# Kernel optimization log

Measured on AMD Instinct MI355X. Metric: run time of the kernel, lower is better.

Reference implementation:

```python
import jax, jax.numpy as jnp
import numpy as np

B, C = 65536, 1000
EPS = float(np.finfo(np.float32).eps)

def setup_inputs() -> dict:
    key = jax.random.key(0)
    k1, k2, k3 = jax.random.split(key, 3)
    return {
        "Simple_vector": jax.random.normal(k1, (B, C), dtype=jnp.float32),
        "label_list": jax.random.randint(k2, (B,), 0, C),
        "w_L": jax.random.normal(k3, (C,), dtype=jnp.float32),
        "w_H": jnp.ones((1,), dtype=jnp.float32),
        "b": jnp.ones((1,), dtype=jnp.float32),
    }

def reference(Simple_vector, label_list, w_L, w_H, b):
    C_ = Simple_vector.shape[1]
    # LTS: per-row dot with class-weight vector
    LTS = Simple_vector @ w_L  # (B,)
    # H_hat = sum_i p_i * log p_i  (negative entropy), single stable pass
    logp = jax.nn.log_softmax(Simple_vector, axis=1)
    H_hat = jnp.sum(jnp.exp(logp) * logp, axis=1)  # (B,)
    HTS = w_H[0] * (H_hat / jnp.log(jnp.float32(C_))) + b[0]
    a = LTS + HTS
    T = jnp.clip(jax.nn.softplus(a), EPS, None)  # (B,)
    scaled = Simple_vector / T[:, None]
    # mean cross-entropy
    ls = jax.nn.log_softmax(scaled, axis=1)
    nll = -jnp.take_along_axis(ls, label_list[:, None], axis=1)[:, 0]
    return jnp.mean(nll)
```

## Files before the change

### kernel.cpp

```cpp
#include <hip/hip_runtime.h>
#include <float.h>
#include <math.h>


static constexpr int   kC4    = 250;
static constexpr int   kBlock = 256;
static constexpr int   kGrid  = 2048;
static constexpr int   kWavesTotal = kGrid * (kBlock / 64);
static constexpr int   kRPW   = 8;
static constexpr float kEps   = 1.1920928955078125e-07f;
static constexpr float kLogC  = 6.907755279f;

__device__ __forceinline__ float wred_max(float v) {
#pragma unroll
  for (int off = 32; off > 0; off >>= 1) v = fmaxf(v, __shfl_xor(v, off, 64));
  return v;
}
__device__ __forceinline__ float wred_sum(float v) {
#pragma unroll
  for (int off = 32; off > 0; off >>= 1) v += __shfl_xor(v, off, 64);
  return v;
}

__device__ __forceinline__ void p1_dot_max(const float4 c, const float4 w,
                                           float& L, float& m) {
  L = fmaf(c.x, w.x, L); L = fmaf(c.y, w.y, L);
  L = fmaf(c.z, w.z, L); L = fmaf(c.w, w.w, L);
  m = fmaxf(m, fmaxf(fmaxf(c.x, c.y), fmaxf(c.z, c.w)));
}
__device__ __forceinline__ void p2_sumexp(const float4 c, const float m,
                                          float& S, float& W) {
  float e;
  e = __expf(c.x - m); S += e; W = fmaf(e, c.x, W);
  e = __expf(c.y - m); S += e; W = fmaf(e, c.y, W);
  e = __expf(c.z - m); S += e; W = fmaf(e, c.z, W);
  e = __expf(c.w - m); S += e; W = fmaf(e, c.w, W);
}
__device__ __forceinline__ void p3_sumexp2(const float4 c, const float rT,
                                           const float nmrT, float& S2) {
  S2 += __expf(fmaf(c.x, rT, nmrT)); S2 += __expf(fmaf(c.y, rT, nmrT));
  S2 += __expf(fmaf(c.z, rT, nmrT)); S2 += __expf(fmaf(c.w, rT, nmrT));
}

#define SENT4 make_float4(-FLT_MAX, -FLT_MAX, -FLT_MAX, -FLT_MAX)

__device__ __forceinline__ float row_nll(
    const float4 c0, const float4 c1, const float4 c2, const float4 c3,
    const float4 w0, const float4 w1, const float4 w2, const float4 w3,
    const int labc, const float wH0, const float b0) {
  float L = 0.f, m = -FLT_MAX;
  p1_dot_max(c0, w0, L, m); p1_dot_max(c1, w1, L, m);
  p1_dot_max(c2, w2, L, m); p1_dot_max(c3, w3, L, m);
  m = wred_max(m);

  float S = 0.f, W = 0.f;
  p2_sumexp(c0, m, S, W); p2_sumexp(c1, m, S, W);
  p2_sumexp(c2, m, S, W); p2_sumexp(c3, m, S, W);
  S = wred_sum(S);
  W = wred_sum(W);
  L = wred_sum(L);

  const int c4l = labc >> 2;
  const int sl  = c4l >> 6, ln = c4l & 63, el = labc & 3;
  float4 v = (sl == 0) ? c0 : (sl == 1) ? c1 : (sl == 2) ? c2 : c3;
  float cand = (el == 0) ? v.x : (el == 1) ? v.y : (el == 2) ? v.z : v.w;
  const float xl = __shfl(cand, ln, 64);

  const float Hhat = W / S - m - __logf(S);
  const float a    = L + wH0 * (Hhat / kLogC) + b0;
  const float sp   = (a > 0.f) ? (a + log1pf(__expf(-a))) : log1pf(__expf(a));
  const float T    = fmaxf(sp, kEps);
  const float rT   = 1.0f / T;
  const float nmrT = -m * rT;

  float S2 = 0.f;
  p3_sumexp2(c0, rT, nmrT, S2); p3_sumexp2(c1, rT, nmrT, S2);
  p3_sumexp2(c2, rT, nmrT, S2); p3_sumexp2(c3, rT, nmrT, S2);
  S2 = wred_sum(S2);

  return __logf(S2) - fmaf(xl, rT, nmrT);
}

__global__ __launch_bounds__(kBlock) void ats_row_kernel_c8(
    const float* __restrict__ X, const int* __restrict__ labels,
    const float* __restrict__ wL, const float* __restrict__ wH,
    const float* __restrict__ bb, double* __restrict__ partial) {
  const int lane   = threadIdx.x & 63;
  const int wib    = threadIdx.x >> 6;
  const int wid    = blockIdx.x * (kBlock / 64) + wib;
  const bool tailok = lane < (kC4 - 192);

  const float4* WLr = reinterpret_cast<const float4*>(wL);
  const float4 w0 = WLr[lane];
  const float4 w1 = WLr[64 + lane];
  const float4 w2 = WLr[128 + lane];
  const float4 w3 = tailok ? WLr[192 + lane] : make_float4(0.f, 0.f, 0.f, 0.f);
  const float wH0 = wH[0];
  const float b0  = bb[0];

  double acc = 0.0;
  const int base = wid * kRPW;

  float4 c0, c1, c2, c3;
  int labc;
  {
    const float4* Xr = reinterpret_cast<const float4*>(X) + (size_t)base * kC4;
    c0 = Xr[lane]; c1 = Xr[64 + lane]; c2 = Xr[128 + lane];
    c3 = tailok ? Xr[192 + lane] : SENT4;
    labc = labels[base];
  }

  for (int i = 0; i < kRPW; ++i) {
    float4 n0 = SENT4, n1 = SENT4, n2 = SENT4, n3 = SENT4;
    int labn = 0;
    if (i + 1 < kRPW) {
      const float4* Xn =
          reinterpret_cast<const float4*>(X) + (size_t)(base + i + 1) * kC4;
      n0 = Xn[lane]; n1 = Xn[64 + lane]; n2 = Xn[128 + lane];
      n3 = tailok ? Xn[192 + lane] : SENT4;
      labn = labels[base + i + 1];
    }

    acc += (double)row_nll(c0, c1, c2, c3, w0, w1, w2, w3, labc, wH0, b0);

    c0 = n0; c1 = n1; c2 = n2; c3 = n3; labc = labn;
  }

  __shared__ double sacc[kBlock / 64];
  if (lane == 0) sacc[wib] = acc;
  __syncthreads();
  if (threadIdx.x == 0)
    partial[blockIdx.x] = (sacc[0] + sacc[1]) + (sacc[2] + sacc[3]);
}

__global__ __launch_bounds__(kBlock) void ats_row_kernel_gen(
    const float* __restrict__ X, const int* __restrict__ labels,
    const float* __restrict__ wL, const float* __restrict__ wH,
    const float* __restrict__ bb, double* __restrict__ partial, int B) {
  const int lane   = threadIdx.x & 63;
  const int wib    = threadIdx.x >> 6;
  const int wid    = blockIdx.x * (kBlock / 64) + wib;
  const bool tailok = lane < (kC4 - 192);

  const float4* WLr = reinterpret_cast<const float4*>(wL);
  const float4 w0 = WLr[lane];
  const float4 w1 = WLr[64 + lane];
  const float4 w2 = WLr[128 + lane];
  const float4 w3 = tailok ? WLr[192 + lane] : make_float4(0.f, 0.f, 0.f, 0.f);
  const float wH0 = wH[0];
  const float b0  = bb[0];

  double acc = 0.0;
  int row = wid;
  float4 c0, c1, c2, c3;
  int labc = 0;
  if (row < B) {
    const float4* Xr = reinterpret_cast<const float4*>(X) + (size_t)row * kC4;
    c0 = Xr[lane]; c1 = Xr[64 + lane]; c2 = Xr[128 + lane];
    c3 = tailok ? Xr[192 + lane] : SENT4;
    labc = labels[row];
  }
  for (; row < B; row += kWavesTotal) {
    const int nrow = row + kWavesTotal;
    float4 n0 = SENT4, n1 = SENT4, n2 = SENT4, n3 = SENT4;
    int labn = 0;
    if (nrow < B) {
      const float4* Xn = reinterpret_cast<const float4*>(X) + (size_t)nrow * kC4;
      n0 = Xn[lane]; n1 = Xn[64 + lane]; n2 = Xn[128 + lane];
      n3 = tailok ? Xn[192 + lane] : SENT4;
      labn = labels[nrow];
    }
    acc += (double)row_nll(c0, c1, c2, c3, w0, w1, w2, w3, labc, wH0, b0);
    c0 = n0; c1 = n1; c2 = n2; c3 = n3; labc = labn;
  }
  __shared__ double sacc[kBlock / 64];
  if (lane == 0) sacc[wib] = acc;
  __syncthreads();
  if (threadIdx.x == 0)
    partial[blockIdx.x] = (sacc[0] + sacc[1]) + (sacc[2] + sacc[3]);
}

__global__ __launch_bounds__(256) void ats_final_kernel(
    const double* __restrict__ partial, float* __restrict__ out, int n, int B) {
  __shared__ double sdata[256];
  double a = 0.0;
  for (int i = threadIdx.x; i < n; i += 256) a += partial[i];
  sdata[threadIdx.x] = a;
  __syncthreads();
#pragma unroll
  for (int s = 128; s > 0; s >>= 1) {
    if ((int)threadIdx.x < s) sdata[threadIdx.x] += sdata[threadIdx.x + s];
    __syncthreads();
  }
  if (threadIdx.x == 0) out[0] = (float)(sdata[0] / (double)B);
}

extern "C" void kernel_launch(void* const* d_in, const int* in_sizes, int n_in,
                              void* d_out, int out_size, void* d_ws, size_t ws_size,
                              hipStream_t stream) {
  (void)n_in; (void)out_size; (void)ws_size;
  const float* X   = (const float*)d_in[0];
  const int*   lab = (const int*)d_in[1];
  const float* wL  = (const float*)d_in[2];
  const float* wH  = (const float*)d_in[3];
  const float* bb  = (const float*)d_in[4];
  const int B = in_sizes[1];
  double* partial = (double*)d_ws;
  float* out = (float*)d_out;

  if (B == kWavesTotal * kRPW) {
    ats_row_kernel_c8<<<kGrid, kBlock, 0, stream>>>(X, lab, wL, wH, bb, partial);
  } else {
    ats_row_kernel_gen<<<kGrid, kBlock, 0, stream>>>(X, lab, wL, wH, bb,
                                                     partial, B);
  }
  ats_final_kernel<<<1, 256, 0, stream>>>(partial, out, kGrid, B);
}
```

Baseline: 63.34 us.

## Fuse final reduction via last-block atomic, use DPP reductions and exp2 math

For the fast path, the final reduction kernel is folded into the row kernel using an atomic counter, so the last block sums the partials, and a memset resets the counter. Wave reductions switch from shuffles to DPP row operations plus readlane. Inputs are prescaled by log2e so the kernel can use native exp2/log2/rcp intrinsics. The generic path loses its prefetch pipelining. The aim is to cut a kernel launch and the shuffle/transcendental instruction cost, at the price of an extra memset launch and slightly different rounding.

```diff
diff --git a/kernel.cpp b/kernel.cpp
--- a/kernel.cpp
+++ b/kernel.cpp
@@ -8,93 +8,106 @@
 static constexpr int   kGrid  = 2048;
 static constexpr int   kWavesTotal = kGrid * (kBlock / 64);
 static constexpr int   kRPW   = 8;
-static constexpr float kEps   = 1.1920928955078125e-07f;
-static constexpr float kLogC  = 6.907755279f;
-
-__device__ __forceinline__ float wred_max(float v) {
-#pragma unroll
-  for (int off = 32; off > 0; off >>= 1) v = fmaxf(v, __shfl_xor(v, off, 64));
-  return v;
-}
-__device__ __forceinline__ float wred_sum(float v) {
-#pragma unroll
-  for (int off = 32; off > 0; off >>= 1) v += __shfl_xor(v, off, 64);
-  return v;
-}
-
-__device__ __forceinline__ void p1_dot_max(const float4 c, const float4 w,
+static constexpr float kEps     = 1.1920928955078125e-07f;
+static constexpr float kInvLogC = 0.14476482730108395f;
+static constexpr float kLn2     = 0.6931471805599453f;
+static constexpr float kLog2e   = 1.4426950408889634f;
+static constexpr float kSent    = -1.7014118e38f;
+
+template <int Ctrl, int Rmask>
+__device__ __forceinline__ float dpp_add(float v) {
+  int t = __builtin_amdgcn_update_dpp(0, __builtin_bit_cast(int, v),
+                                      Ctrl, Rmask, 0xf, false);
+  return v + __builtin_bit_cast(float, t);
+}
+template <int Ctrl, int Rmask>
+__device__ __forceinline__ float dpp_max(float v) {
+  int t = __builtin_amdgcn_update_dpp((int)0xFF800000,
+                                      __builtin_bit_cast(int, v),
+                                      Ctrl, Rmask, 0xf, false);
+  return fmaxf(v, __builtin_bit_cast(float, t));
+}
+__device__ __forceinline__ float bcast63(float v) {
+  return __builtin_bit_cast(
+      float, __builtin_amdgcn_readlane(__builtin_bit_cast(int, v), 63));
+}
+__device__ __forceinline__ float wred_sum_dpp(float v) {
+  v = dpp_add<0xB1, 0xF>(v);
+  v = dpp_add<0x4E, 0xF>(v);
+  v = dpp_add<0x141, 0xF>(v);
+  v = dpp_add<0x140, 0xF>(v);
+  v = dpp_add<0x142, 0xA>(v);
+  v = dpp_add<0x143, 0xC>(v);
+  return bcast63(v);
+}
+__device__ __forceinline__ float wred_max_dpp(float v) {
+  v = dpp_max<0xB1, 0xF>(v);
+  v = dpp_max<0x4E, 0xF>(v);
+  v = dpp_max<0x141, 0xF>(v);
+  v = dpp_max<0x140, 0xF>(v);
+  v = dpp_max<0x142, 0xA>(v);
+  v = dpp_max<0x143, 0xC>(v);
+  return bcast63(v);
+}
+__device__ __forceinline__ void wred_sum3_dpp(float& a, float& b, float& c) {
+  a = dpp_add<0xB1, 0xF>(a);  b = dpp_add<0xB1, 0xF>(b);  c = dpp_add<0xB1, 0xF>(c);
+  a = dpp_add<0x4E, 0xF>(a);  b = dpp_add<0x4E, 0xF>(b);  c = dpp_add<0x4E, 0xF>(c);
+  a = dpp_add<0x141, 0xF>(a); b = dpp_add<0x141, 0xF>(b); c = dpp_add<0x141, 0xF>(c);
+  a = dpp_add<0x140, 0xF>(a); b = dpp_add<0x140, 0xF>(b); c = dpp_add<0x140, 0xF>(c);
+  a = dpp_add<0x142, 0xA>(a); b = dpp_add<0x142, 0xA>(b); c = dpp_add<0x142, 0xA>(c);
+  a = dpp_add<0x143, 0xC>(a); b = dpp_add<0x143, 0xC>(b); c = dpp_add<0x143, 0xC>(c);
+  a = bcast63(a); b = bcast63(b); c = bcast63(c);
+}
+
+__device__ __forceinline__ void scale4(float4& c) {
+  c.x *= kLog2e; c.y *= kLog2e; c.z *= kLog2e; c.w *= kLog2e;
+}
+__device__ __forceinline__ void p1_dot_max(const float4 y, const float4 w,
                                            float& L, float& m) {
-  L = fmaf(c.x, w.x, L); L = fmaf(c.y, w.y, L);
-  L = fmaf(c.z, w.z, L); L = fmaf(c.w, w.w, L);
-  m = fmaxf(m, fmaxf(fmaxf(c.x, c.y), fmaxf(c.z, c.w)));
-}
-__device__ __forceinline__ void p2_sumexp(const float4 c, const float m,
-                                          float& S, float& W) {
+  L = fmaf(y.x, w.x, L); L = fmaf(y.y, w.y, L);
+  L = fmaf(y.z, w.z, L); L = fmaf(y.w, w.w, L);
+  m = fmaxf(m, fmaxf(fmaxf(y.x, y.y), fmaxf(y.z, y.w)));
+}
+__device__ __forceinline__ void p2_sumexp(const float4 y, const float my,
+                                          float& S, float& Wp) {
   float e;
-  e = __expf(c.x - m); S += e; W = fmaf(e, c.x, W);
-  e = __expf(c.y - m); S += e; W = fmaf(e, c.y, W);
-  e = __expf(c.z - m); S += e; W = fmaf(e, c.z, W);
-  e = __expf(c.w - m); S += e; W = fmaf(e, c.w, W);
-}
-__device__ __forceinline__ void p3_sumexp2(const float4 c, const float rT,
-                                           const float nmrT, float& S2) {
-  S2 += __expf(fmaf(c.x, rT, nmrT)); S2 += __expf(fmaf(c.y, rT, nmrT));
-  S2 += __expf(fmaf(c.z, rT, nmrT)); S2 += __expf(fmaf(c.w, rT, nmrT));
-}
-
-#define SENT4 make_float4(-FLT_MAX, -FLT_MAX, -FLT_MAX, -FLT_MAX)
-
-__device__ __forceinline__ float row_nll(
-    const float4 c0, const float4 c1, const float4 c2, const float4 c3,
-    const float4 w0, const float4 w1, const float4 w2, const float4 w3,
-    const int labc, const float wH0, const float b0) {
-  float L = 0.f, m = -FLT_MAX;
-  p1_dot_max(c0, w0, L, m); p1_dot_max(c1, w1, L, m);
-  p1_dot_max(c2, w2, L, m); p1_dot_max(c3, w3, L, m);
-  m = wred_max(m);
-
-  float S = 0.f, W = 0.f;
-  p2_sumexp(c0, m, S, W); p2_sumexp(c1, m, S, W);
-  p2_sumexp(c2, m, S, W); p2_sumexp(c3, m, S, W);
-  S = wred_sum(S);
-  W = wred_sum(W);
-  L = wred_sum(L);
-
-  const int c4l = labc >> 2;
-  const int sl  = c4l >> 6, ln = c4l & 63, el = labc & 3;
-  float4 v = (sl == 0) ? c0 : (sl == 1) ? c1 : (sl == 2) ? c2 : c3;
-  float cand = (el == 0) ? v.x : (el == 1) ? v.y : (el == 2) ? v.z : v.w;
-  const float xl = __shfl(cand, ln, 64);
-
-  const float Hhat = W / S - m - __logf(S);
-  const float a    = L + wH0 * (Hhat / kLogC) + b0;
-  const float sp   = (a > 0.f) ? (a + log1pf(__expf(-a))) : log1pf(__expf(a));
-  const float T    = fmaxf(sp, kEps);
-  const float rT   = 1.0f / T;
-  const float nmrT = -m * rT;
-
-  float S2 = 0.f;
-  p3_sumexp2(c0, rT, nmrT, S2); p3_sumexp2(c1, rT, nmrT, S2);
-  p3_sumexp2(c2, rT, nmrT, S2); p3_sumexp2(c3, rT, nmrT, S2);
-  S2 = wred_sum(S2);
-
-  return __logf(S2) - fmaf(xl, rT, nmrT);
-}
+  e = __builtin_amdgcn_exp2f(y.x - my); S += e; Wp = fmaf(e, y.x, Wp);
+  e = __builtin_amdgcn_exp2f(y.y - my); S += e; Wp = fmaf(e, y.y, Wp);
+  e = __builtin_amdgcn_exp2f(y.z - my); S += e; Wp = fmaf(e, y.z, Wp);
+  e = __builtin_amdgcn_exp2f(y.w - my); S += e; Wp = fmaf(e, y.w, Wp);
+}
+__device__ __forceinline__ void p3_sumexp2(const float4 y, const float rT,
+                                           const float nmy, float& S2) {
+  S2 += __builtin_amdgcn_exp2f(fmaf(y.x, rT, nmy));
+  S2 += __builtin_amdgcn_exp2f(fmaf(y.y, rT, nmy));
+  S2 += __builtin_amdgcn_exp2f(fmaf(y.z, rT, nmy));
+  S2 += __builtin_amdgcn_exp2f(fmaf(y.w, rT, nmy));
+}
+__device__ __forceinline__ float pick_lab(const float4 v, const int el) {
+  return (el == 0) ? v.x : (el == 1) ? v.y : (el == 2) ? v.z : v.w;
+}
+
+#define SENT4 make_float4(kSent, kSent, kSent, kSent)
 
 __global__ __launch_bounds__(kBlock) void ats_row_kernel_c8(
     const float* __restrict__ X, const int* __restrict__ labels,
     const float* __restrict__ wL, const float* __restrict__ wH,
-    const float* __restrict__ bb, double* __restrict__ partial) {
+    const float* __restrict__ bb, double* __restrict__ partial,
+    unsigned* __restrict__ counter, float* __restrict__ out, int B) {
   const int lane   = threadIdx.x & 63;
   const int wib    = threadIdx.x >> 6;
   const int wid    = blockIdx.x * (kBlock / 64) + wib;
   const bool tailok = lane < (kC4 - 192);
 
   const float4* WLr = reinterpret_cast<const float4*>(wL);
-  const float4 w0 = WLr[lane];
-  const float4 w1 = WLr[64 + lane];
-  const float4 w2 = WLr[128 + lane];
-  const float4 w3 = tailok ? WLr[192 + lane] : make_float4(0.f, 0.f, 0.f, 0.f);
+  float4 w0 = WLr[lane];
+  float4 w1 = WLr[64 + lane];
+  float4 w2 = WLr[128 + lane];
+  float4 w3 = tailok ? WLr[192 + lane] : make_float4(0.f, 0.f, 0.f, 0.f);
+  w0.x *= kLn2; w0.y *= kLn2; w0.z *= kLn2; w0.w *= kLn2;
+  w1.x *= kLn2; w1.y *= kLn2; w1.z *= kLn2; w1.w *= kLn2;
+  w2.x *= kLn2; w2.y *= kLn2; w2.z *= kLn2; w2.w *= kLn2;
+  w3.x *= kLn2; w3.y *= kLn2; w3.z *= kLn2; w3.w *= kLn2;
   const float wH0 = wH[0];
   const float b0  = bb[0];
 
@@ -121,18 +134,82 @@
       labn = labels[base + i + 1];
     }
 
-    acc += (double)row_nll(c0, c1, c2, c3, w0, w1, w2, w3, labc, wH0, b0);
+    scale4(c0); scale4(c1); scale4(c2); scale4(c3);
+
+    float L = 0.f, my = -FLT_MAX;
+    p1_dot_max(c0, w0, L, my); p1_dot_max(c1, w1, L, my);
+    p1_dot_max(c2, w2, L, my); p1_dot_max(c3, w3, L, my);
+    my = wred_max_dpp(my);
+
+    float S = 0.f, Wp = 0.f;
+    p2_sumexp(c0, my, S, Wp); p2_sumexp(c1, my, S, Wp);
+    p2_sumexp(c2, my, S, Wp); p2_sumexp(c3, my, S, Wp);
+    wred_sum3_dpp(S, Wp, L);
+
+    const int c4l = labc >> 2;
+    const int sl  = c4l >> 6, ln = c4l & 63, el = labc & 3;
+    float4 v = (sl == 0) ? c0 : (sl == 1) ? c1 : (sl == 2) ? c2 : c3;
+    const float yl = __shfl(pick_lab(v, el), ln, 64);
+
+    const float rcpS = __builtin_amdgcn_rcpf(S);
+    const float Hhat = kLn2 * (Wp * rcpS - my - __builtin_amdgcn_logf(S));
+    const float a    = L + fmaf(wH0, Hhat * kInvLogC, b0);
+    const float sp   = (a > 0.f) ? (a + log1pf(__expf(-a))) : log1pf(__expf(a));
+    const float T    = fmaxf(sp, kEps);
+    const float rT   = __builtin_amdgcn_rcpf(T);
+    const float nmy  = -my * rT;
+
+    float S2 = 0.f;
+    p3_sumexp2(c0, rT, nmy, S2); p3_sumexp2(c1, rT, nmy, S2);
+    p3_sumexp2(c2, rT, nmy, S2); p3_sumexp2(c3, rT, nmy, S2);
+    S2 = wred_sum_dpp(S2);
+
+    const float nll = kLn2 * (__builtin_amdgcn_logf(S2) - fmaf(yl, rT, nmy));
+    acc += (double)nll;
 
     c0 = n0; c1 = n1; c2 = n2; c3 = n3; labc = labn;
   }
 
   __shared__ double sacc[kBlock / 64];
+  __shared__ unsigned slast;
   if (lane == 0) sacc[wib] = acc;
   __syncthreads();
-  if (threadIdx.x == 0)
-    partial[blockIdx.x] = (sacc[0] + sacc[1]) + (sacc[2] + sacc[3]);
-}
-
+  if (threadIdx.x == 0) {
+    const double p = (sacc[0] + sacc[1]) + (sacc[2] + sacc[3]);
+    __hip_atomic_store(&partial[blockIdx.x], p, __ATOMIC_RELEASE,
+                       __HIP_MEMORY_SCOPE_AGENT);
+    const unsigned prev = __hip_atomic_fetch_add(
+        counter, 1u, __ATOMIC_ACQ_REL, __HIP_MEMORY_SCOPE_AGENT);
+    slast = (prev == (unsigned)(gridDim.x - 1)) ? 1u : 0u;
+  }
+  __syncthreads();
+  if (slast) {
+    double a = 0.0;
+    for (int i = threadIdx.x; i < kGrid; i += kBlock)
+      a += __hip_atomic_load(&partial[i], __ATOMIC_RELAXED,
+                             __HIP_MEMORY_SCOPE_AGENT);
+    __shared__ double sred[kBlock];
+    sred[threadIdx.x] = a;
+    __syncthreads();
+#pragma unroll
+    for (int s = kBlock / 2; s > 0; s >>= 1) {
+      if ((int)threadIdx.x < s) sred[threadIdx.x] += sred[threadIdx.x + s];
+      __syncthreads();
+    }
+    if (threadIdx.x == 0) out[0] = (float)(sred[0] / (double)B);
+  }
+}
+
+__device__ __forceinline__ float wred_sum_shfl(float v) {
+#pragma unroll
+  for (int off = 32; off > 0; off >>= 1) v += __shfl_xor(v, off, 64);
+  return v;
+}
+__device__ __forceinline__ float wred_max_shfl(float v) {
+#pragma unroll
+  for (int off = 32; off > 0; off >>= 1) v = fmaxf(v, __shfl_xor(v, off, 64));
+  return v;
+}
 __global__ __launch_bounds__(kBlock) void ats_row_kernel_gen(
     const float* __restrict__ X, const int* __restrict__ labels,
     const float* __restrict__ wL, const float* __restrict__ wH,
@@ -151,27 +228,67 @@
   const float b0  = bb[0];
 
   double acc = 0.0;
-  int row = wid;
-  float4 c0, c1, c2, c3;
-  int labc = 0;
-  if (row < B) {
+  for (int row = wid; row < B; row += kWavesTotal) {
     const float4* Xr = reinterpret_cast<const float4*>(X) + (size_t)row * kC4;
-    c0 = Xr[lane]; c1 = Xr[64 + lane]; c2 = Xr[128 + lane];
-    c3 = tailok ? Xr[192 + lane] : SENT4;
-    labc = labels[row];
-  }
-  for (; row < B; row += kWavesTotal) {
-    const int nrow = row + kWavesTotal;
-    float4 n0 = SENT4, n1 = SENT4, n2 = SENT4, n3 = SENT4;
-    int labn = 0;
-    if (nrow < B) {
-      const float4* Xn = reinterpret_cast<const float4*>(X) + (size_t)nrow * kC4;
-      n0 = Xn[lane]; n1 = Xn[64 + lane]; n2 = Xn[128 + lane];
-      n3 = tailok ? Xn[192 + lane] : SENT4;
-      labn = labels[nrow];
+    float4 c0 = Xr[lane], c1 = Xr[64 + lane], c2 = Xr[128 + lane];
+    float4 c3 = tailok ? Xr[192 + lane] : SENT4;
+    const int labc = labels[row];
+
+    float L = 0.f, m = -FLT_MAX;
+    float S = 0.f, W = 0.f;
+    {
+      float e;
+      L = fmaf(c0.x, w0.x, L); L = fmaf(c0.y, w0.y, L);
+      L = fmaf(c0.z, w0.z, L); L = fmaf(c0.w, w0.w, L);
+      m = fmaxf(m, fmaxf(fmaxf(c0.x, c0.y), fmaxf(c0.z, c0.w)));
+      L = fmaf(c1.x, w1.x, L); L = fmaf(c1.y, w1.y, L);
+      L = fmaf(c1.z, w1.z, L); L = fmaf(c1.w, w1.w, L);
+      m = fmaxf(m, fmaxf(fmaxf(c1.x, c1.y), fmaxf(c1.z, c1.w)));
+      L = fmaf(c2.x, w2.x, L); L = fmaf(c2.y, w2.y, L);
+      L = fmaf(c2.z, w2.z, L); L = fmaf(c2.w, w2.w, L);
+      m = fmaxf(m, fmaxf(fmaxf(c2.x, c2.y), fmaxf(c2.z, c2.w)));
+      L = fmaf(c3.x, w3.x, L); L = fmaf(c3.y, w3.y, L);
+      L = fmaf(c3.z, w3.z, L); L = fmaf(c3.w, w3.w, L);
+      m = fmaxf(m, fmaxf(fmaxf(c3.x, c3.y), fmaxf(c3.z, c3.w)));
+      m = wred_max_shfl(m);
+      e = __expf(c0.x - m); S += e; W = fmaf(e, c0.x, W);
+      e = __expf(c0.y - m); S += e; W = fmaf(e, c0.y, W);
+      e = __expf(c0.z - m); S += e; W = fmaf(e, c0.z, W);
+      e = __expf(c0.w - m); S += e; W = fmaf(e, c0.w, W);
+      e = __expf(c1.x - m); S += e; W = fmaf(e, c1.x, W);
+      e = __expf(c1.y - m); S += e; W = fmaf(e, c1.y, W);
+      e = __expf(c1.z - m); S += e; W = fmaf(e, c1.z, W);
+      e = __expf(c1.w - m); S += e; W = fmaf(e, c1.w, W);
+      e = __expf(c2.x - m); S += e; W = fmaf(e, c2.x, W);
+      e = __expf(c2.y - m); S += e; W = fmaf(e, c2.y, W);
+      e = __expf(c2.z - m); S += e; W = fmaf(e, c2.z, W);
+      e = __expf(c2.w - m); S += e; W = fmaf(e, c2.w, W);
+      e = __expf(c3.x - m); S += e; W = fmaf(e, c3.x, W);
+      e = __expf(c3.y - m); S += e; W = fmaf(e, c3.y, W);
+      e = __expf(c3.z - m); S += e; W = fmaf(e, c3.z, W);
+      e = __expf(c3.w - m); S += e; W = fmaf(e, c3.w, W);
+      S = wred_sum_shfl(S); W = wred_sum_shfl(W); L = wred_sum_shfl(L);
     }
-    acc += (double)row_nll(c0, c1, c2, c3, w0, w1, w2, w3, labc, wH0, b0);
-    c0 = n0; c1 = n1; c2 = n2; c3 = n3; labc = labn;
+    const int c4l = labc >> 2;
+    const int sl = c4l >> 6, ln = c4l & 63, el = labc & 3;
+    float4 v = (sl == 0) ? c0 : (sl == 1) ? c1 : (sl == 2) ? c2 : c3;
+    const float xl = __shfl(pick_lab(v, el), ln, 64);
+    const float Hhat = W / S - m - __logf(S);
+    const float a = L + wH0 * (Hhat * kInvLogC) + b0;
+    const float sp = (a > 0.f) ? (a + log1pf(__expf(-a))) : log1pf(__expf(a));
+    const float T = fmaxf(sp, kEps);
+    const float rT = 1.0f / T, nmrT = -m * rT;
+    float S2 = 0.f;
+    S2 += __expf(fmaf(c0.x, rT, nmrT)); S2 += __expf(fmaf(c0.y, rT, nmrT));
+    S2 += __expf(fmaf(c0.z, rT, nmrT)); S2 += __expf(fmaf(c0.w, rT, nmrT));
+    S2 += __expf(fmaf(c1.x, rT, nmrT)); S2 += __expf(fmaf(c1.y, rT, nmrT));
+    S2 += __expf(fmaf(c1.z, rT, nmrT)); S2 += __expf(fmaf(c1.w, rT, nmrT));
+    S2 += __expf(fmaf(c2.x, rT, nmrT)); S2 += __expf(fmaf(c2.y, rT, nmrT));
+    S2 += __expf(fmaf(c2.z, rT, nmrT)); S2 += __expf(fmaf(c2.w, rT, nmrT));
+    S2 += __expf(fmaf(c3.x, rT, nmrT)); S2 += __expf(fmaf(c3.y, rT, nmrT));
+    S2 += __expf(fmaf(c3.z, rT, nmrT)); S2 += __expf(fmaf(c3.w, rT, nmrT));
+    S2 = wred_sum_shfl(S2);
+    acc += (double)(__logf(S2) - fmaf(xl, rT, nmrT));
   }
   __shared__ double sacc[kBlock / 64];
   if (lane == 0) sacc[wib] = acc;
@@ -205,14 +322,17 @@
   const float* wH  = (const float*)d_in[3];
   const float* bb  = (const float*)d_in[4];
   const int B = in_sizes[1];
-  double* partial = (double*)d_ws;
-  float* out = (float*)d_out;
+  unsigned* counter = (unsigned*)d_ws;
+  double*   partial = (double*)((char*)d_ws + 256);
+  float*    out     = (float*)d_out;
 
   if (B == kWavesTotal * kRPW) {
-    ats_row_kernel_c8<<<kGrid, kBlock, 0, stream>>>(X, lab, wL, wH, bb, partial);
+    hipMemsetAsync(d_ws, 0, 4, stream);
+    ats_row_kernel_c8<<<kGrid, kBlock, 0, stream>>>(X, lab, wL, wH, bb,
+                                                    partial, counter, out, B);
   } else {
     ats_row_kernel_gen<<<kGrid, kBlock, 0, stream>>>(X, lab, wL, wH, bb,
                                                      partial, B);
-  }
-  ats_final_kernel<<<1, 256, 0, stream>>>(partial, out, kGrid, B);
-}
+    ats_final_kernel<<<1, 256, 0, stream>>>(partial, out, kGrid, B);
+  }
+}
```

Result: slower. 185.1 us (+192.3%).
